# Kernel optimization log

Measured on AMD Instinct MI355X. Metric: run time of the kernel, lower is better.

The kernel has to match this reference:

```python
import jax, jax.numpy as jnp
import numpy as np

E = 16        # n_experts
K = 2         # n_active_experts
D = 2048      # d_model
F = 1408      # ffn_hidden
B, S = 4, 2048


def _swiglu(x, wg, wu, wd):
    # x: [N, D]; wg/wu: [F, D]; wd: [D, F]
    return (jax.nn.silu(x @ wg.T) * (x @ wu.T)) @ wd.T


def setup_inputs() -> dict:
    key = jax.random.key(0)
    ks = jax.random.split(key, 8)
    sc = 0.02
    return {
        "x": jax.random.normal(ks[0], (B, S, D), jnp.float32),
        "gate_w": jax.random.normal(ks[1], (E, D), jnp.float32) * sc,
        "w_gate": jax.random.normal(ks[2], (E, F, D), jnp.float32) * sc,
        "w_up": jax.random.normal(ks[3], (E, F, D), jnp.float32) * sc,
        "w_down": jax.random.normal(ks[4], (E, D, F), jnp.float32) * sc,
        "sw_gate": jax.random.normal(ks[5], (F, D), jnp.float32) * sc,
        "sw_up": jax.random.normal(ks[6], (F, D), jnp.float32) * sc,
        "sw_down": jax.random.normal(ks[7], (D, F), jnp.float32) * sc,
        "expert_bias": jnp.zeros((E,), jnp.float32),
    }


def reference(x, gate_w, w_gate, w_up, w_down, sw_gate, sw_up, sw_down, expert_bias):
    b, s, d = x.shape
    flat = x.reshape(-1, d)                           # [N, D]
    logits = flat @ gate_w.T                          # [N, E]
    probs = jax.nn.softmax(logits, axis=-1)
    biased = logits + expert_bias
    _, top_idx = jax.lax.top_k(biased, K)             # [N, K] int32
    top_w = jnp.take_along_axis(probs, top_idx, axis=-1)
    top_w = top_w / jnp.sum(top_w, axis=-1, keepdims=True)
    # scatter top-k weights into a dense per-expert combine matrix [N, E]
    combine = jnp.sum(jax.nn.one_hot(top_idx, E, dtype=flat.dtype) * top_w[..., None], axis=1)
    out = jnp.zeros_like(flat)
    for e in range(E):  # fixed small expert loop
        out = out + combine[:, e:e + 1] * _swiglu(flat, w_gate[e], w_up[e], w_down[e])
    out = out + _swiglu(flat, sw_gate, sw_up, sw_down)  # shared expert
    return out.reshape(b, s, d)
```

## Files before the change

kernel.cpp:

```cpp
#include <hip/hip_runtime.h>
#include <hip/hip_bf16.h>
#include <cstdint>

#define NE 16
#define D_ 2048
#define F_ 1408
#define NTOK 8192
#define NPAIR (NTOK * 2)
#define SHARED_BASE NPAIR
#define NTOT (NPAIR + NTOK)

#define BM1 256
#define BN1 128
#define BN2 256
#define BK 64
#define NF1 (F_ / BN1)
#define NF2 (D_ / BN2)
#define MAXRT 111
#define GEMMB1 (MAXRT * NF1)
#define CVTB 512

typedef __attribute__((ext_vector_type(8))) short short8;
typedef __attribute__((ext_vector_type(4))) float f32x4;

static __device__ __forceinline__ ushort f2bf(float f) {
    union { float f; unsigned u; } v; v.f = f;
    unsigned u = v.u;
    return (ushort)((u + 0x7FFFu + ((u >> 16) & 1u)) >> 16);
}

static __device__ __forceinline__ float bf2f(ushort u) {
    union { unsigned u; float f; } v; v.u = ((unsigned)u) << 16;
    return v.f;
}

static __device__ __forceinline__ void cvt_store8(ushort* dst, const float* src) {
    const float4* s = reinterpret_cast<const float4*>(src);
    float4 a = s[0], b = s[1];
    short8 v;
    v[0] = (short)f2bf(a.x); v[1] = (short)f2bf(a.y);
    v[2] = (short)f2bf(a.z); v[3] = (short)f2bf(a.w);
    v[4] = (short)f2bf(b.x); v[5] = (short)f2bf(b.y);
    v[6] = (short)f2bf(b.z); v[7] = (short)f2bf(b.w);
    *reinterpret_cast<short8*>(dst) = v;
}

static __device__ __forceinline__ void gll16(const void* g, void* l) {
    __builtin_amdgcn_global_load_lds((const __attribute__((address_space(1))) void*)g,
                                     (__attribute__((address_space(3))) void*)l, 16, 0, 0);
}

static __device__ __forceinline__ int xcd_map(int p, int nwg) {
    int q = nwg >> 3, r = nwg & 7;
    int x = p & 7, k = p >> 3;
    int base = (x < r) ? x * (q + 1) : r * (q + 1) + (x - r) * q;
    return base + k;
}

__global__ __launch_bounds__(256) void k_cvt(const float* __restrict__ src,
                                             ushort* __restrict__ dst, int n8) {
    int i = blockIdx.x * 256 + threadIdx.x;
    int stride = gridDim.x * 256;
    for (; i < n8; i += stride) cvt_store8(dst + (size_t)i * 8, src + (size_t)i * 8);
}

__global__ __launch_bounds__(256) void k_route(const float* __restrict__ x,
                                               const float* __restrict__ gate_w,
                                               const float* __restrict__ expert_bias,
                                               int* __restrict__ topk_idx,
                                               float* __restrict__ topk_w) {
    const int wave = threadIdx.x >> 6;
    const int lane = threadIdx.x & 63;
    const int tok = blockIdx.x * 4 + wave;
    if (tok >= NTOK) return;
    const float* xr = x + (size_t)tok * D_;
    float xv[D_ / 64];
#pragma unroll
    for (int i = 0; i < D_ / 64; ++i) xv[i] = xr[lane + 64 * i];

    float logits[NE];
#pragma unroll
    for (int e = 0; e < NE; ++e) {
        const float* gw = gate_w + e * D_;
        float p = 0.f;
#pragma unroll
        for (int i = 0; i < D_ / 64; ++i) p += xv[i] * gw[lane + 64 * i];
#pragma unroll
        for (int off = 32; off > 0; off >>= 1) p += __shfl_xor(p, off, 64);
        logits[e] = p;
    }
    int i1 = 0; float b1 = logits[0] + expert_bias[0];
#pragma unroll
    for (int e = 1; e < NE; ++e) {
        float b = logits[e] + expert_bias[e];
        if (b > b1) { b1 = b; i1 = e; }
    }
    int i2 = -1; float b2 = -3.4e38f;
#pragma unroll
    for (int e = 0; e < NE; ++e) {
        if (e == i1) continue;
        float b = logits[e] + expert_bias[e];
        if (b > b2) { b2 = b; i2 = e; }
    }
    float l1 = logits[i1], l2 = logits[i2];
    float m = fmaxf(l1, l2);
    float e1 = __expf(l1 - m), e2 = __expf(l2 - m);
    float s = e1 + e2;
    if (lane == 0) {
        topk_idx[tok * 2 + 0] = i1;
        topk_idx[tok * 2 + 1] = i2;
        topk_w[tok * 2 + 0] = e1 / s;
        topk_w[tok * 2 + 1] = e2 / s;
    }
}

__global__ void k_zero_meta(int* meta) {
    if (threadIdx.x < 128) meta[threadIdx.x] = 0;
}

__global__ __launch_bounds__(256) void k_count(const int* __restrict__ topk_idx,
                                               int* __restrict__ meta) {
    int t = blockIdx.x * 256 + threadIdx.x;
    if (t >= NTOK) return;
    atomicAdd(&meta[topk_idx[t * 2 + 0]], 1);
    atomicAdd(&meta[topk_idx[t * 2 + 1]], 1);
}

__global__ void k_prefix(int* meta) {
    if (threadIdx.x == 0) {
        int acc = 0;
        for (int e = 0; e < NE; ++e) { meta[32 + e] = acc; acc += meta[e]; }
        meta[32 + NE] = acc;
        int t = 0;
        for (int e = 0; e < NE; ++e) { meta[64 + e] = t; t += (meta[e] + BM1 - 1) / BM1; }
        meta[64 + NE] = t;
        meta[64 + NE + 1] = t + NTOK / BM1;
    }
}

__global__ __launch_bounds__(256) void k_scatter(const int* __restrict__ topk_idx,
                                                 const float* __restrict__ topk_w,
                                                 int* __restrict__ meta,
                                                 int* __restrict__ tok_sorted,
                                                 float* __restrict__ w_sorted,
                                                 int* __restrict__ inv) {
    int t = blockIdx.x * 256 + threadIdx.x;
    if (t >= NTOK) return;
#pragma unroll
    for (int k = 0; k < 2; ++k) {
        int e = topk_idx[t * 2 + k];
        int p = atomicAdd(&meta[16 + e], 1);
        int idx = meta[32 + e] + p;
        tok_sorted[idx] = t;
        w_sorted[idx] = topk_w[t * 2 + k];
        inv[t * 2 + k] = idx;
    }
}

static __device__ __forceinline__ bool grid_decode(const int* meta, int bid, int NF,
                                                   int& e, int& row0, int& fx) {
    if (bid >= meta[64 + NE + 1] * NF) return false;
    e = (bid >= meta[64 + NE] * NF) ? NE : 0;
    if (e == 0) {
#pragma unroll
        for (int i = 1; i < NE; ++i) if (bid >= meta[64 + i] * NF) e = i;
    }
    const int tile_base = meta[64 + e];
    const int nrt = meta[64 + e + 1] - tile_base;
    const int bw = bid - tile_base * NF;
    fx = bw / nrt;
    row0 = (bw - fx * nrt) * BM1;
    return true;
}

__global__ __launch_bounds__(512, 2) void k_ffn1(const ushort* __restrict__ xb,
                                                 const ushort* __restrict__ wgb,
                                                 const ushort* __restrict__ wub,
                                                 const ushort* __restrict__ swgb,
                                                 const ushort* __restrict__ swub,
                                                 const int* __restrict__ meta,
                                                 const int* __restrict__ tok_sorted,
                                                 const float* __restrict__ w_sorted,
                                                 ushort* __restrict__ Hbuf,
                                                 const float* __restrict__ w_down,
                                                 const float* __restrict__ sw_down,
                                                 ushort* __restrict__ wdb,
                                                 ushort* __restrict__ swdb) {
    const int tid = threadIdx.x;
    if (blockIdx.x >= GEMMB1) {
        const int NW8 = NE * F_ * D_ / 8;
        const int NSW8 = F_ * D_ / 8;
        int ci = (blockIdx.x - GEMMB1) * 512 + tid;
        const int cstride = CVTB * 512;
        for (; ci < NW8 + NSW8; ci += cstride) {
            if (ci < NW8) cvt_store8(wdb + (size_t)ci * 8, w_down + (size_t)ci * 8);
            else {
                int j = ci - NW8;
                cvt_store8(swdb + (size_t)j * 8, sw_down + (size_t)j * 8);
            }
        }
        return;
    }

    int e, row0, fx;
    const int lbid = xcd_map(blockIdx.x, GEMMB1);
    if (!grid_decode(meta, lbid, NF1, e, row0, fx)) return;
    int n_e, base;
    if (e < NE) { n_e = meta[e]; base = meta[32 + e]; }
    else        { n_e = NTOK;    base = SHARED_BASE; }
    const int f0 = fx * BN1;
    const ushort* wg = (e < NE) ? wgb + (size_t)e * F_ * D_ : swgb;
    const ushort* wu = (e < NE) ? wub + (size_t)e * F_ * D_ : swub;

    __shared__ __align__(16) ushort As[2][BM1 * BK];
    __shared__ __align__(16) ushort Gs[2][BN1 * BK];
    __shared__ __align__(16) ushort Us[2][BN1 * BK];
    __shared__ int tks[BM1];
    __shared__ float tws[BM1];

    const int wv = tid >> 6, lane = tid & 63;
    if (tid < BM1) {
        int r = row0 + tid;
        if (r < n_e) {
            tks[tid] = (e < NE) ? tok_sorted[base + r] : r;
            tws[tid] = (e < NE) ? w_sorted[base + r] : 1.0f;
        } else { tks[tid] = 0; tws[tid] = 0.f; }
    }
    __syncthreads();

    const ushort* srcA[4]; const ushort* srcG[2]; const ushort* srcU[2];
#pragma unroll
    for (int j = 0; j < 4; ++j) {
        int c = j * 512 + wv * 64 + lane;
        int r = c >> 3;
        int col = ((c & 7) ^ (r & 7)) * 8;
        srcA[j] = xb + (size_t)tks[r] * D_ + col;
    }
#pragma unroll
    for (int j = 0; j < 2; ++j) {
        int c = j * 512 + wv * 64 + lane;
        int r = c >> 3;
        int col = ((c & 7) ^ (r & 7)) * 8;
        srcG[j] = wg + (size_t)(f0 + r) * D_ + col;
        srcU[j] = wu + (size_t)(f0 + r) * D_ + col;
    }

    auto stage = [&](int buf, int k0) {
        char* bA = (char*)(&As[buf][0]) + wv * 1024;
        char* bG = (char*)(&Gs[buf][0]) + wv * 1024;
        char* bU = (char*)(&Us[buf][0]) + wv * 1024;
        gll16(srcA[0] + k0, bA);         gll16(srcA[1] + k0, bA + 8192);
        gll16(srcA[2] + k0, bA + 16384); gll16(srcA[3] + k0, bA + 24576);
        gll16(srcG[0] + k0, bG);         gll16(srcG[1] + k0, bG + 8192);
        gll16(srcU[0] + k0, bU);         gll16(srcU[1] + k0, bU + 8192);
    };

    f32x4 accg[4][4] = {}; f32x4 accu[4][4] = {};
    const int wm = (wv >> 1) * 64, wn = (wv & 1) * 64;
    const int fr = lane & 15, fq = lane >> 4;
    const int sw = fr & 7;
    const int rc0 = ((fq ^ sw) * 8);
    const int rc1 = (((4 + fq) ^ sw) * 8);

    auto compute = [&](int buf) {
        const ushort* pA = As[buf];
        const ushort* pG = Gs[buf];
        const ushort* pU = Us[buf];
#pragma unroll
        for (int kk = 0; kk < 2; ++kk) {
            const int rc = kk ? rc1 : rc0;
            short8 af[4], gf[4], uf[4];
#pragma unroll
            for (int mi = 0; mi < 4; ++mi)
                af[mi] = *reinterpret_cast<const short8*>(&pA[(wm + mi * 16 + fr) * BK + rc]);
#pragma unroll
            for (int ni = 0; ni < 4; ++ni) {
                gf[ni] = *reinterpret_cast<const short8*>(&pG[(wn + ni * 16 + fr) * BK + rc]);
                uf[ni] = *reinterpret_cast<const short8*>(&pU[(wn + ni * 16 + fr) * BK + rc]);
            }
#pragma unroll
            for (int mi = 0; mi < 4; ++mi)
#pragma unroll
                for (int ni = 0; ni < 4; ++ni) {
                    accg[mi][ni] = __builtin_amdgcn_mfma_f32_16x16x32_bf16(af[mi], gf[ni], accg[mi][ni], 0, 0, 0);
                    accu[mi][ni] = __builtin_amdgcn_mfma_f32_16x16x32_bf16(af[mi], uf[ni], accu[mi][ni], 0, 0, 0);
                }
        }
    };

    const int NK = D_ / BK;
    stage(0, 0);
    stage(1, BK);
    asm volatile("s_waitcnt vmcnt(8)" ::: "memory");
    __builtin_amdgcn_s_barrier();
    __builtin_amdgcn_sched_barrier(0);
    int cur = 0;
    for (int ks = 0; ks < NK; ++ks) {
        compute(cur);
        __builtin_amdgcn_s_barrier();
        if (ks + 2 < NK) {
            stage(cur, (ks + 2) * BK);
            asm volatile("s_waitcnt vmcnt(8)" ::: "memory");
        } else if (ks + 1 < NK) {
            asm volatile("s_waitcnt vmcnt(0)" ::: "memory");
        }
        __builtin_amdgcn_s_barrier();
        __builtin_amdgcn_sched_barrier(0);
        cur ^= 1;
    }

#pragma unroll
    for (int mi = 0; mi < 4; ++mi) {
#pragma unroll
        for (int r = 0; r < 4; ++r) {
            int lr = wm + mi * 16 + fq * 4 + r;
            int grow = row0 + lr;
            if (grow < n_e) {
                float w = tws[lr];
                ushort* hrow = Hbuf + (size_t)(base + grow) * F_ + f0 + wn;
#pragma unroll
                for (int ni = 0; ni < 4; ++ni) {
                    float g = accg[mi][ni][r];
                    float u = accu[mi][ni][r];
                    float h = w * (g / (1.f + __expf(-g))) * u;
                    hrow[ni * 16 + fr] = f2bf(h);
                }
            }
        }
    }
}

__global__ __launch_bounds__(512, 2) void k_ffn2(const ushort* __restrict__ Hbuf,
                                                 const ushort* __restrict__ wdb,
                                                 const ushort* __restrict__ swdb,
                                                 const int* __restrict__ meta,
                                                 ushort* __restrict__ Obuf) {
    int e, row0, dx;
    if (!grid_decode(meta, blockIdx.x, NF2, e, row0, dx)) return;
    int n_e, base;
    if (e < NE) { n_e = meta[e]; base = meta[32 + e]; }
    else        { n_e = NTOK;    base = SHARED_BASE; }
    const int d0 = dx * BN2;
    const ushort* wd = (e < NE) ? wdb + (size_t)e * D_ * F_ : swdb;

    __shared__ __align__(16) ushort As[2][BM1 * BK];
    __shared__ __align__(16) ushort Bs[2][BN2 * BK];

    const int tid = threadIdx.x;
    const int wv = tid >> 6, lane = tid & 63;

    const ushort* srcA[4]; const ushort* srcB[4];
#pragma unroll
    for (int j = 0; j < 4; ++j) {
        int c = j * 512 + wv * 64 + lane;
        int r = c >> 3;
        int col = ((c & 7) ^ (r & 7)) * 8;
        srcA[j] = Hbuf + (size_t)(base + row0 + r) * F_ + col;
        srcB[j] = wd + (size_t)(d0 + r) * F_ + col;
    }

    auto stage = [&](int buf, int k0) {
        char* bA = (char*)(&As[buf][0]) + wv * 1024;
        char* bB = (char*)(&Bs[buf][0]) + wv * 1024;
        gll16(srcA[0] + k0, bA);         gll16(srcA[1] + k0, bA + 8192);
        gll16(srcA[2] + k0, bA + 16384); gll16(srcA[3] + k0, bA + 24576);
        gll16(srcB[0] + k0, bB);         gll16(srcB[1] + k0, bB + 8192);
        gll16(srcB[2] + k0, bB + 16384); gll16(srcB[3] + k0, bB + 24576);
    };

    f32x4 acc[4][8] = {};
    const int wm = (wv >> 1) * 64, wn = (wv & 1) * 128;
    const int fr = lane & 15, fq = lane >> 4;
    const int sw = fr & 7;
    const int rc0 = ((fq ^ sw) * 8);
    const int rc1 = (((4 + fq) ^ sw) * 8);

    auto compute = [&](int buf) {
        const ushort* pA = As[buf];
        const ushort* pB = Bs[buf];
#pragma unroll
        for (int kk = 0; kk < 2; ++kk) {
            const int rc = kk ? rc1 : rc0;
            short8 af[4], bfr[8];
#pragma unroll
            for (int mi = 0; mi < 4; ++mi)
                af[mi] = *reinterpret_cast<const short8*>(&pA[(wm + mi * 16 + fr) * BK + rc]);
#pragma unroll
            for (int ni = 0; ni < 8; ++ni)
                bfr[ni] = *reinterpret_cast<const short8*>(&pB[(wn + ni * 16 + fr) * BK + rc]);
#pragma unroll
            for (int mi = 0; mi < 4; ++mi)
#pragma unroll
                for (int ni = 0; ni < 8; ++ni)
                    acc[mi][ni] = __builtin_amdgcn_mfma_f32_16x16x32_bf16(af[mi], bfr[ni], acc[mi][ni], 0, 0, 0);
        }
    };

    const int NK = F_ / BK;
    stage(0, 0);
    stage(1, BK);
    asm volatile("s_waitcnt vmcnt(8)" ::: "memory");
    __builtin_amdgcn_s_barrier();
    __builtin_amdgcn_sched_barrier(0);
    int cur = 0;
    for (int ks = 0; ks < NK; ++ks) {
        compute(cur);
        __builtin_amdgcn_s_barrier();
        if (ks + 2 < NK) {
            stage(cur, (ks + 2) * BK);
            asm volatile("s_waitcnt vmcnt(8)" ::: "memory");
        } else if (ks + 1 < NK) {
            asm volatile("s_waitcnt vmcnt(0)" ::: "memory");
        }
        __builtin_amdgcn_s_barrier();
        __builtin_amdgcn_sched_barrier(0);
        cur ^= 1;
    }

#pragma unroll
    for (int mi = 0; mi < 4; ++mi) {
#pragma unroll
        for (int r = 0; r < 4; ++r) {
            int lr = wm + mi * 16 + fq * 4 + r;
            int slot = row0 + lr;
            if (slot < n_e) {
                ushort* orow = Obuf + (size_t)(base + slot) * D_ + d0 + wn;
#pragma unroll
                for (int ni = 0; ni < 8; ++ni)
                    orow[ni * 16 + fr] = f2bf(acc[mi][ni][r]);
            }
        }
    }
}

__global__ __launch_bounds__(256) void k_gather(const ushort* __restrict__ Obuf,
                                                const int* __restrict__ inv,
                                                float* __restrict__ out) {
    const int t = blockIdx.x;
    const int c = threadIdx.x * 8;
    const int s1 = inv[t * 2 + 0];
    const int s2 = inv[t * 2 + 1];
    short8 a = *reinterpret_cast<const short8*>(&Obuf[(size_t)s1 * D_ + c]);
    short8 b = *reinterpret_cast<const short8*>(&Obuf[(size_t)s2 * D_ + c]);
    short8 d = *reinterpret_cast<const short8*>(&Obuf[(size_t)(SHARED_BASE + t) * D_ + c]);
    float4 o0, o1;
    o0.x = bf2f((ushort)a[0]) + bf2f((ushort)b[0]) + bf2f((ushort)d[0]);
    o0.y = bf2f((ushort)a[1]) + bf2f((ushort)b[1]) + bf2f((ushort)d[1]);
    o0.z = bf2f((ushort)a[2]) + bf2f((ushort)b[2]) + bf2f((ushort)d[2]);
    o0.w = bf2f((ushort)a[3]) + bf2f((ushort)b[3]) + bf2f((ushort)d[3]);
    o1.x = bf2f((ushort)a[4]) + bf2f((ushort)b[4]) + bf2f((ushort)d[4]);
    o1.y = bf2f((ushort)a[5]) + bf2f((ushort)b[5]) + bf2f((ushort)d[5]);
    o1.z = bf2f((ushort)a[6]) + bf2f((ushort)b[6]) + bf2f((ushort)d[6]);
    o1.w = bf2f((ushort)a[7]) + bf2f((ushort)b[7]) + bf2f((ushort)d[7]);
    float4* op = reinterpret_cast<float4*>(out + (size_t)t * D_ + c);
    op[0] = o0; op[1] = o1;
}

extern "C" void kernel_launch(void* const* d_in, const int* in_sizes, int n_in,
                              void* d_out, int out_size, void* d_ws, size_t ws_size,
                              hipStream_t stream) {
    const float* x        = (const float*)d_in[0];
    const float* gate_w   = (const float*)d_in[1];
    const float* w_gate   = (const float*)d_in[2];
    const float* w_up     = (const float*)d_in[3];
    const float* w_down   = (const float*)d_in[4];
    const float* sw_gate  = (const float*)d_in[5];
    const float* sw_up    = (const float*)d_in[6];
    const float* sw_down  = (const float*)d_in[7];
    const float* expert_bias = (const float*)d_in[8];
    float* out = (float*)d_out;

    const size_t NW = (size_t)NE * F_ * D_;
    const size_t NSW = (size_t)F_ * D_;
    const size_t NX = (size_t)NTOK * D_;

    char* ws = (char*)d_ws;
    size_t off = 0;
    ushort* xb   = (ushort*)(ws + off); off += NX * 2;
    ushort* wgb  = (ushort*)(ws + off); off += NW * 2;
    ushort* wub  = (ushort*)(ws + off); off += NW * 2;
    ushort* wdb  = (ushort*)(ws + off); off += NW * 2;
    ushort* swgb = (ushort*)(ws + off); off += NSW * 2;
    ushort* swub = (ushort*)(ws + off); off += NSW * 2;
    ushort* swdb = (ushort*)(ws + off); off += NSW * 2;
    ushort* Hbuf = (ushort*)(ws + off); off += (size_t)NTOT * F_ * 2;
    int* tok_sorted = (int*)(ws + off); off += NPAIR * sizeof(int);
    float* w_sorted = (float*)(ws + off); off += NPAIR * sizeof(float);
    int* topk_idx = (int*)(ws + off); off += NTOK * 2 * sizeof(int);
    float* topk_w = (float*)(ws + off); off += NTOK * 2 * sizeof(float);
    int* inv = (int*)(ws + off); off += NTOK * 2 * sizeof(int);
    int* meta = (int*)(ws + off); off += 512;

    ushort* Obuf = wgb;

    k_route<<<NTOK / 4, 256, 0, stream>>>(x, gate_w, expert_bias, topk_idx, topk_w);
    k_zero_meta<<<1, 128, 0, stream>>>(meta);
    k_count<<<NTOK / 256, 256, 0, stream>>>(topk_idx, meta);
    k_prefix<<<1, 1, 0, stream>>>(meta);
    k_scatter<<<NTOK / 256, 256, 0, stream>>>(topk_idx, topk_w, meta, tok_sorted, w_sorted, inv);

    auto cvt = [&](const float* s, ushort* d, size_t n) {
        int n8 = (int)(n / 8);
        int blocks = (n8 + 255) / 256;
        if (blocks > 4096) blocks = 4096;
        k_cvt<<<blocks, 256, 0, stream>>>(s, d, n8);
    };
    cvt(x, xb, NX);
    cvt(w_gate, wgb, NW);
    cvt(w_up, wub, NW);
    cvt(sw_gate, swgb, NSW);
    cvt(sw_up, swub, NSW);

    k_ffn1<<<GEMMB1 + CVTB, 512, 0, stream>>>(xb, wgb, wub, swgb, swub,
                                              meta, tok_sorted, w_sorted, Hbuf,
                                              w_down, sw_down, wdb, swdb);

    k_ffn2<<<MAXRT * NF2, 512, 0, stream>>>(Hbuf, wdb, swdb, meta, Obuf);

    k_gather<<<NTOK, 256, 0, stream>>>(Obuf, inv, out);
}
```

Before: 879.3 us.

## Fuse bf16 conversions into routing kernel and XCD-remap ffn2 blocks

```diff
diff --git a/kernel.cpp b/kernel.cpp
--- a/kernel.cpp
+++ b/kernel.cpp
@@ -19,6 +19,8 @@
 #define MAXRT 111
 #define GEMMB1 (MAXRT * NF1)
 #define CVTB 512
+#define ROUTEB (NTOK / 4)
+#define CVTB2 2048
 
 typedef __attribute__((ext_vector_type(8))) short short8;
 typedef __attribute__((ext_vector_type(4))) float f32x4;
@@ -57,18 +59,42 @@
     return base + k;
 }
 
-__global__ __launch_bounds__(256) void k_cvt(const float* __restrict__ src,
-                                             ushort* __restrict__ dst, int n8) {
-    int i = blockIdx.x * 256 + threadIdx.x;
-    int stride = gridDim.x * 256;
-    for (; i < n8; i += stride) cvt_store8(dst + (size_t)i * 8, src + (size_t)i * 8);
-}
-
 __global__ __launch_bounds__(256) void k_route(const float* __restrict__ x,
                                                const float* __restrict__ gate_w,
                                                const float* __restrict__ expert_bias,
                                                int* __restrict__ topk_idx,
-                                               float* __restrict__ topk_w) {
+                                               float* __restrict__ topk_w,
+                                               const float* __restrict__ w_gate,
+                                               const float* __restrict__ w_up,
+                                               const float* __restrict__ sw_gate,
+                                               const float* __restrict__ sw_up,
+                                               ushort* __restrict__ xb,
+                                               ushort* __restrict__ wgb,
+                                               ushort* __restrict__ wub,
+                                               ushort* __restrict__ swgb,
+                                               ushort* __restrict__ swub) {
+    if (blockIdx.x >= ROUTEB) {
+        const int NX8 = NTOK * D_ / 8;
+        const int NW8 = NE * F_ * D_ / 8;
+        const int NSW8 = F_ * D_ / 8;
+        const int TOT = NX8 + 2 * NW8 + 2 * NSW8;
+        int ci = (blockIdx.x - ROUTEB) * 256 + threadIdx.x;
+        const int cstride = CVTB2 * 256;
+        for (; ci < TOT; ci += cstride) {
+            int j = ci;
+            if (j < NX8) { cvt_store8(xb + (size_t)j * 8, x + (size_t)j * 8); continue; }
+            j -= NX8;
+            if (j < NW8) { cvt_store8(wgb + (size_t)j * 8, w_gate + (size_t)j * 8); continue; }
+            j -= NW8;
+            if (j < NW8) { cvt_store8(wub + (size_t)j * 8, w_up + (size_t)j * 8); continue; }
+            j -= NW8;
+            if (j < NSW8) { cvt_store8(swgb + (size_t)j * 8, sw_gate + (size_t)j * 8); continue; }
+            j -= NSW8;
+            cvt_store8(swub + (size_t)j * 8, sw_up + (size_t)j * 8);
+        }
+        return;
+    }
+
     const int wave = threadIdx.x >> 6;
     const int lane = threadIdx.x & 63;
     const int tok = blockIdx.x * 4 + wave;
@@ -336,7 +362,8 @@
                                                  const int* __restrict__ meta,
                                                  ushort* __restrict__ Obuf) {
     int e, row0, dx;
-    if (!grid_decode(meta, blockIdx.x, NF2, e, row0, dx)) return;
+    const int lbid = xcd_map(blockIdx.x, gridDim.x);
+    if (!grid_decode(meta, lbid, NF2, e, row0, dx)) return;
     int n_e, base;
     if (e < NE) { n_e = meta[e]; base = meta[32 + e]; }
     else        { n_e = NTOK;    base = SHARED_BASE; }
@@ -493,24 +520,14 @@
 
     ushort* Obuf = wgb;
 
-    k_route<<<NTOK / 4, 256, 0, stream>>>(x, gate_w, expert_bias, topk_idx, topk_w);
+    k_route<<<ROUTEB + CVTB2, 256, 0, stream>>>(x, gate_w, expert_bias, topk_idx, topk_w,
+                                                w_gate, w_up, sw_gate, sw_up,
+                                                xb, wgb, wub, swgb, swub);
     k_zero_meta<<<1, 128, 0, stream>>>(meta);
     k_count<<<NTOK / 256, 256, 0, stream>>>(topk_idx, meta);
     k_prefix<<<1, 1, 0, stream>>>(meta);
     k_scatter<<<NTOK / 256, 256, 0, stream>>>(topk_idx, topk_w, meta, tok_sorted, w_sorted, inv);
 
-    auto cvt = [&](const float* s, ushort* d, size_t n) {
-        int n8 = (int)(n / 8);
-        int blocks = (n8 + 255) / 256;
-        if (blocks > 4096) blocks = 4096;
-        k_cvt<<<blocks, 256, 0, stream>>>(s, d, n8);
-    };
-    cvt(x, xb, NX);
-    cvt(w_gate, wgb, NW);
-    cvt(w_up, wub, NW);
-    cvt(sw_gate, swgb, NSW);
-    cvt(sw_up, swub, NSW);
-
     k_ffn1<<<GEMMB1 + CVTB, 512, 0, stream>>>(xb, wgb, wub, swgb, swub,
                                               meta, tok_sorted, w_sorted, Hbuf,
                                               w_down, sw_down, wdb, swdb);
```

Measured after the change: 872.3 us (median of 2 runs). Within noise of the previous version (-0.8%).
